# Performance work log

Measured on AMD Instinct MI355X. Metric: run time of the kernel, lower is better.

The kernel has to match this reference:

```python
import jax, jax.numpy as jnp
import numpy as np

NH, NKV, HD = 16, 4, 128
ROPE_THETA = 10000.0


def setup_inputs() -> dict:
    key = jax.random.key(0)
    ks = jax.random.split(key, 5)
    std = jnp.float32(0.02)
    return {
        "hidden_states": jax.random.normal(ks[0], (1, 2048, 2048), jnp.float32),
        "wq": jax.random.normal(ks[1], (2048, NH * HD), jnp.float32) * std,
        "wk": jax.random.normal(ks[2], (2048, NKV * HD), jnp.float32) * std,
        "wv": jax.random.normal(ks[3], (2048, NKV * HD), jnp.float32) * std,
        "wo": jax.random.normal(ks[4], (NH * HD, 2048), jnp.float32) * std,
    }


def _rope(x, cos, sin):
    # x: [B,S,n,hd]; pairs (even,odd) treated as complex, multiplied by cis(angle)
    xr = x.reshape(*x.shape[:-1], HD // 2, 2)
    re, im = xr[..., 0], xr[..., 1]
    c = cos[None, :, None, :]  # [1,S,1,hd/2]
    s = sin[None, :, None, :]
    out = jnp.stack((re * c - im * s, re * s + im * c), axis=-1)
    return out.reshape(x.shape)


def reference(hidden_states, wq, wk, wv, wo):
    B, S, H = hidden_states.shape
    q = (hidden_states @ wq).reshape(B, S, NH, HD)
    k = (hidden_states @ wk).reshape(B, S, NKV, HD)
    v = (hidden_states @ wv).reshape(B, S, NKV, HD)

    # precompute_freqs_cis (full rotary dim, rot_dim=None)
    freqs = 1.0 / (ROPE_THETA ** (jnp.arange(0, HD, 2, dtype=jnp.float32) / HD))
    ang = jnp.outer(jnp.arange(S, dtype=jnp.float32), freqs)  # [S, hd/2]
    cos, sin = jnp.cos(ang), jnp.sin(ang)

    q = _rope(q.astype(jnp.float32), cos, sin)
    k = _rope(k.astype(jnp.float32), cos, sin)

    # GQA: repeat_kv == repeat_interleave over head axis
    n_rep = NH // NKV
    k = jnp.repeat(k, n_rep, axis=2)  # [B,S,NH,HD]
    v = jnp.repeat(v, n_rep, axis=2)

    scale = jnp.float32(1.0 / np.sqrt(HD))
    scores = jnp.einsum("bqhd,bkhd->bhqk", q, k) * scale
    causal = jnp.tril(jnp.ones((S, S), dtype=bool))
    scores = jnp.where(causal[None, None], scores, jnp.float32(-1e9))
    attn = jax.nn.softmax(scores, axis=-1)
    out = jnp.einsum("bhqk,bkhd->bqhd", attn, v).reshape(B, S, NH * HD)
    return out @ wo
```

## Files before the change

kernel.cpp:

```cpp
#include <hip/hip_runtime.h>
#include <cstdint>

typedef __attribute__((ext_vector_type(8))) short short8;
typedef __attribute__((ext_vector_type(4))) float f32x4;

static __device__ __forceinline__ unsigned short f2bf(float x) {
  union { float f; unsigned int u; } c; c.f = x;
  unsigned int u = c.u;
  unsigned int r = (u + 0x7fffu + ((u >> 16) & 1u)) >> 16;
  return (unsigned short)r;
}

static __device__ __forceinline__ void gl_lds16(const void* g, void* l) {
  __builtin_amdgcn_global_load_lds((const __attribute__((address_space(1))) void*)g,
                                   (__attribute__((address_space(3))) void*)l, 16, 0, 0);
}

__global__ __launch_bounds__(256) void k_f32_to_bf16(const float* __restrict__ src,
                                                     unsigned short* __restrict__ dst,
                                                     int n4) {
  int i = blockIdx.x * 256 + threadIdx.x;
  if (i >= n4) return;
  float4 v = reinterpret_cast<const float4*>(src)[i];
  ushort4 o;
  o.x = f2bf(v.x); o.y = f2bf(v.y); o.z = f2bf(v.z); o.w = f2bf(v.w);
  reinterpret_cast<ushort4*>(dst)[i] = o;
}

__global__ __launch_bounds__(256) void k_transpose_bf16(const float* __restrict__ src,
                                                        unsigned short* __restrict__ dst,
                                                        int K, int N, int sstride) {
  __shared__ float tile[32][33];
  int bn = blockIdx.x * 32, bk = blockIdx.y * 32;
  int tx = threadIdx.x & 31, ty = threadIdx.x >> 5;
#pragma unroll
  for (int i = 0; i < 32; i += 8)
    tile[ty + i][tx] = src[(size_t)(bk + ty + i) * sstride + bn + tx];
  __syncthreads();
#pragma unroll
  for (int i = 0; i < 32; i += 8)
    dst[(size_t)(bn + ty + i) * K + bk + tx] = f2bf(tile[tx][ty + i]);
}

__global__ __launch_bounds__(256) void k_transpose_all(const float* __restrict__ wq,
                                                       const float* __restrict__ wk,
                                                       const float* __restrict__ wv,
                                                       const float* __restrict__ wo,
                                                       unsigned short* __restrict__ wqt,
                                                       unsigned short* __restrict__ wkt,
                                                       unsigned short* __restrict__ wvt,
                                                       unsigned short* __restrict__ wot) {
  __shared__ float tile[32][33];
  int id = blockIdx.x;
  const float* src; unsigned short* dst; int N, t;
  if (id < 4096)       { src = wq; dst = wqt; N = 2048; t = id; }
  else if (id < 8192)  { src = wo; dst = wot; N = 2048; t = id - 4096; }
  else if (id < 9216)  { src = wk; dst = wkt; N = 512;  t = id - 8192; }
  else                 { src = wv; dst = wvt; N = 512;  t = id - 9216; }
  const int K = 2048;
  int ntx = N >> 5;
  int bn = (t % ntx) * 32, bk = (t / ntx) * 32;
  int tx = threadIdx.x & 31, ty = threadIdx.x >> 5;
#pragma unroll
  for (int i = 0; i < 32; i += 8)
    tile[ty + i][tx] = src[(size_t)(bk + ty + i) * N + bn + tx];
  __syncthreads();
#pragma unroll
  for (int i = 0; i < 32; i += 8)
    dst[(size_t)(bn + ty + i) * K + bk + tx] = f2bf(tile[tx][ty + i]);
}

__global__ __launch_bounds__(256) void k_rope_fused(const float* __restrict__ qkvf,
                                                    unsigned short* __restrict__ qd,
                                                    unsigned short* __restrict__ kd) {
  int idx = blockIdx.x * 256 + threadIdx.x;
  int i = idx & 63;
  int hh = (idx >> 6) % 20;
  int s = idx / (64 * 20);
  float freq = powf(10000.0f, -(float)i / 64.0f);
  float ang = (float)s * freq;
  float sn, cs;
  sincosf(ang, &sn, &cs);
  size_t sb; unsigned short* dp; float amp;
  if (hh < 16) {
    int col = hh * 128 + 2 * i;
    sb = (size_t)s * 3072 + col;
    dp = qd + (size_t)s * 2048 + col;
    amp = 0.12751742836257666f;
  } else {
    int col = (hh - 16) * 128 + 2 * i;
    sb = (size_t)s * 3072 + 2048 + col;
    dp = kd + (size_t)s * 512 + col;
    amp = 1.0f;
  }
  float re = qkvf[sb] * amp, im = qkvf[sb + 1] * amp;
  unsigned int lo = f2bf(re * cs - im * sn);
  unsigned int hi = f2bf(re * sn + im * cs);
  *(unsigned int*)dp = lo | (hi << 16);
}

__global__ __launch_bounds__(256) void k_gemm_bf16(const unsigned short* __restrict__ A,
                                                   const unsigned short* __restrict__ Bt,
                                                   float* __restrict__ C,
                                                   int M, int N, int K) {
  __shared__ short sA[2][128 * 64];
  __shared__ short sB[2][64 * 64];
  int tid = threadIdx.x;
  int lane = tid & 63, wid = tid >> 6;
  int wr = wid >> 1, wc = wid & 1;

  int gx = gridDim.x, nwg = gx * gridDim.y;
  int flat = blockIdx.y * gx + blockIdx.x;
  int l = (flat & 7) * (nwg >> 3) + (flat >> 3);
  int bx = l % gx, by = l / gx;
  int m0 = by * 128, n0 = bx * 64;

  f32x4 acc[4][2] = {};

  int srcCol = (((tid & 7) ^ ((tid >> 3) & 7)) << 3);
  int rA = tid >> 3;
  const unsigned short* Ag = A + (size_t)(m0 + rA) * K + srcCol;
  const unsigned short* Bg = Bt + (size_t)(n0 + rA) * K + srcCol;
  int wb = (tid & ~63) * 8;

  int g = lane >> 4, fr = lane & 15, sw = fr & 7;

#define STAGE_G(buf, kof) do { \
    gl_lds16(Ag + (kof),                    &sA[buf][wb]); \
    gl_lds16(Ag + 32 * (size_t)K + (kof),   &sA[buf][2048 + wb]); \
    gl_lds16(Ag + 64 * (size_t)K + (kof),   &sA[buf][4096 + wb]); \
    gl_lds16(Ag + 96 * (size_t)K + (kof),   &sA[buf][6144 + wb]); \
    gl_lds16(Bg + (kof),                    &sB[buf][wb]); \
    gl_lds16(Bg + 32 * (size_t)K + (kof),   &sB[buf][2048 + wb]); \
  } while (0)

  int nt = K >> 6;
  STAGE_G(0, 0);
  __syncthreads();

  int cur = 0;
  for (int t = 0; t < nt; t++) {
    if (t + 1 < nt) STAGE_G(cur ^ 1, (size_t)((t + 1) << 6));
    const short* sAc = sA[cur];
    const short* sBc = sB[cur];
#pragma unroll
    for (int kk = 0; kk < 2; kk++) {
      int so = ((((kk << 2) + g) ^ sw) << 3);
      short8 af[4], bf2[2];
#pragma unroll
      for (int x = 0; x < 4; x++)
        af[x] = *(const short8*)(sAc + (wr * 64 + x * 16 + fr) * 64 + so);
#pragma unroll
      for (int ni = 0; ni < 2; ni++)
        bf2[ni] = *(const short8*)(sBc + (wc * 32 + ni * 16 + fr) * 64 + so);
#pragma unroll
      for (int x = 0; x < 4; x++)
#pragma unroll
        for (int ni = 0; ni < 2; ni++)
          acc[x][ni] = __builtin_amdgcn_mfma_f32_16x16x32_bf16(af[x], bf2[ni], acc[x][ni], 0, 0, 0);
    }
    __syncthreads();
    cur ^= 1;
  }
#undef STAGE_G

  int col = n0 + wc * 32 + fr;
  int rb = m0 + wr * 64 + (g << 2);
#pragma unroll
  for (int x = 0; x < 4; x++)
#pragma unroll
    for (int ni = 0; ni < 2; ni++)
#pragma unroll
      for (int j = 0; j < 4; j++)
        C[(size_t)(rb + x * 16 + j) * N + col + ni * 16] = acc[x][ni][j];
}

#define KSTR 136
#define VSTR 72
#define PSTR 72
__global__ __launch_bounds__(256) void k_attn_mfma(const unsigned short* __restrict__ Qb,
                                                   const unsigned short* __restrict__ Kb,
                                                   const unsigned short* __restrict__ Vt,
                                                   unsigned short* __restrict__ O) {
  __shared__ short sK[2][64 * KSTR];
  __shared__ short sV[2][128 * VSTR];
  __shared__ short sP[4][16 * PSTR];
  int h = blockIdx.y;
  int x = blockIdx.x;
  int qb = (h < 8) ? x : (31 - x);
  int q0 = qb * 64;
  int kvh = h >> 2;
  int tid = threadIdx.x, lane = tid & 63, w = tid >> 6;
  int fr = lane & 15, g = lane >> 4, kq = g << 3;

  short8 qf[4];
  {
    const unsigned short* qrow = Qb + (size_t)(q0 + w * 16 + fr) * 2048 + h * 128 + kq;
#pragma unroll
    for (int ko = 0; ko < 4; ko++) qf[ko] = *(const short8*)(qrow + ko * 32);
  }

  f32x4 oacc[8];
#pragma unroll
  for (int nd = 0; nd < 8; nd++) oacc[nd] = (f32x4){0.f, 0.f, 0.f, 0.f};
  float m_i = -3e38f;
  float l_i = 0.f;

  int skr = tid >> 2, skc = (tid & 3) << 5;
  int svd = tid >> 1, svc = (tid & 1) << 5;
  const unsigned short* Kbase = Kb + (size_t)kvh * 128 + skc;
  const unsigned short* Vbase = Vt + (size_t)(kvh * 128 + svd) * 2048 + svc;
  short* pw = (short*)sP[w];
  int kdOff = skr * KSTR + skc;
  int vdOff = svd * VSTR + svc;

  short8 kreg[4], vreg[4];
  {
    const short8* ks = (const short8*)(Kbase + (size_t)skr * 512);
    const short8* vs = (const short8*)(Vbase);
#pragma unroll
    for (int j = 0; j < 4; j++) { kreg[j] = ks[j]; vreg[j] = vs[j]; }
  }
  {
    short* kd = sK[0] + kdOff; short* vd = sV[0] + vdOff;
#pragma unroll
    for (int j = 0; j < 4; j++) { *(short8*)(kd + j * 8) = kreg[j]; *(short8*)(vd + j * 8) = vreg[j]; }
  }
  if (qb >= 1) {
    const short8* ks = (const short8*)(Kbase + (size_t)(64 + skr) * 512);
    const short8* vs = (const short8*)(Vbase + 64);
#pragma unroll
    for (int j = 0; j < 4; j++) { kreg[j] = ks[j]; vreg[j] = vs[j]; }
  }
  __syncthreads();

  int qrowS = q0 + w * 16 + fr;

  for (int kt = 0; kt <= qb; kt++) {
    int c = kt & 1;
    const short* sKc = sK[c];
    const short* sVc = sV[c];

    f32x4 sacc[4];
#pragma unroll
    for (int ni = 0; ni < 4; ni++) sacc[ni] = (f32x4){0.f, 0.f, 0.f, 0.f};
    __builtin_amdgcn_s_setprio(1);
#pragma unroll
    for (int ko = 0; ko < 4; ko++)
#pragma unroll
      for (int ni = 0; ni < 4; ni++) {
        short8 kf = *(const short8*)(sKc + (ni * 16 + fr) * KSTR + kq + ko * 32);
        sacc[ni] = __builtin_amdgcn_mfma_f32_16x16x32_bf16(kf, qf[ko], sacc[ni], 0, 0, 0);
      }
    __builtin_amdgcn_s_setprio(0);

    if (kt == qb) {
      int k0 = kt * 64;
#pragma unroll
      for (int ni = 0; ni < 4; ni++) {
        int kc = k0 + ni * 16 + (g << 2);
#pragma unroll
        for (int j = 0; j < 4; j++)
          if (kc + j > qrowS) sacc[ni][j] = -3e38f;
      }
    }

    float tm = sacc[0][0];
#pragma unroll
    for (int ni = 0; ni < 4; ni++)
#pragma unroll
      for (int j = 0; j < 4; j++) tm = fmaxf(tm, sacc[ni][j]);
    tm = fmaxf(tm, __shfl_xor(tm, 16));
    tm = fmaxf(tm, __shfl_xor(tm, 32));

    if (!__all(tm <= m_i + 8.0f)) {
      float mn = fmaxf(m_i, tm);
      float sc = exp2f(m_i - mn);
      m_i = mn;
      float scj[4];
#pragma unroll
      for (int j = 0; j < 4; j++) scj[j] = __shfl(sc, (g << 2) + j);
#pragma unroll
      for (int nd = 0; nd < 8; nd++)
#pragma unroll
        for (int j = 0; j < 4; j++) oacc[nd][j] *= scj[j];
      l_i *= sc;
    }

    float ps = 0.f;
#pragma unroll
    for (int ni = 0; ni < 4; ni++) {
      float p0 = exp2f(sacc[ni][0] - m_i);
      float p1 = exp2f(sacc[ni][1] - m_i);
      float p2 = exp2f(sacc[ni][2] - m_i);
      float p3 = exp2f(sacc[ni][3] - m_i);
      ps += (p0 + p1) + (p2 + p3);
      ushort4 pk;
      pk.x = f2bf(p0); pk.y = f2bf(p1); pk.z = f2bf(p2); pk.w = f2bf(p3);
      *(ushort4*)(pw + fr * PSTR + ni * 16 + (g << 2)) = pk;
    }
    ps += __shfl_xor(ps, 16);
    ps += __shfl_xor(ps, 32);
    l_i += ps;

    __builtin_amdgcn_s_setprio(1);
#pragma unroll
    for (int ks = 0; ks < 2; ks++) {
      short8 pa = *(const short8*)(pw + fr * PSTR + kq + ks * 32);
#pragma unroll
      for (int nd = 0; nd < 8; nd++) {
        short8 vb = *(const short8*)(sVc + (nd * 16 + fr) * VSTR + kq + ks * 32);
        oacc[nd] = __builtin_amdgcn_mfma_f32_16x16x32_bf16(pa, vb, oacc[nd], 0, 0, 0);
      }
    }
    __builtin_amdgcn_s_setprio(0);

    if (kt < qb) {
      short* kd = sK[c ^ 1] + kdOff; short* vd = sV[c ^ 1] + vdOff;
#pragma unroll
      for (int j = 0; j < 4; j++) { *(short8*)(kd + j * 8) = kreg[j]; *(short8*)(vd + j * 8) = vreg[j]; }
      if (kt + 1 < qb) {
        int k2 = (kt + 2) * 64;
        const short8* ks = (const short8*)(Kbase + (size_t)(k2 + skr) * 512);
        const short8* vs = (const short8*)(Vbase + k2);
#pragma unroll
        for (int j = 0; j < 4; j++) { kreg[j] = ks[j]; vreg[j] = vs[j]; }
      }
      __syncthreads();
    }
  }

  int orow = q0 + w * 16 + (g << 2);
#pragma unroll
  for (int j = 0; j < 4; j++) {
    float lj = __shfl(l_i, (g << 2) + j);
    float inv = 1.0f / lj;
#pragma unroll
    for (int nd = 0; nd < 8; nd++)
      O[(size_t)(orow + j) * 2048 + h * 128 + nd * 16 + fr] = f2bf(oacc[nd][j] * inv);
  }
}

extern "C" void kernel_launch(void* const* d_in, const int* in_sizes, int n_in,
                              void* d_out, int out_size, void* d_ws, size_t ws_size,
                              hipStream_t stream) {
  const float* hs = (const float*)d_in[0];
  const float* wq = (const float*)d_in[1];
  const float* wk = (const float*)d_in[2];
  const float* wv = (const float*)d_in[3];
  const float* wo = (const float*)d_in[4];
  char* ws = (char*)d_ws;

  unsigned short* hb   = (unsigned short*)(ws);
  unsigned short* wqt  = (unsigned short*)(ws + 8388608);
  unsigned short* wkt  = (unsigned short*)(ws + 16777216);
  unsigned short* wvt  = (unsigned short*)(ws + 18874368);
  unsigned short* wot  = (unsigned short*)(ws + 20971520);
  float* qkvf          = (float*)(ws + 29360128);
  unsigned short* q_bf = wqt;
  unsigned short* k_bf = wkt;
  unsigned short* vt_bf = wvt;
  unsigned short* ao   = hb;
  float* out = (float*)d_out;

  k_f32_to_bf16<<<4096, 256, 0, stream>>>(hs, hb, 2048 * 2048 / 4);
  k_transpose_all<<<10240, 256, 0, stream>>>(wq, wk, wv, wo, wqt, wkt, wvt, wot);

  k_gemm_bf16<<<dim3(48, 16), 256, 0, stream>>>(hb, wqt, qkvf, 2048, 3072, 2048);

  k_rope_fused<<<10240, 256, 0, stream>>>(qkvf, q_bf, k_bf);
  k_transpose_bf16<<<dim3(16, 64), 256, 0, stream>>>(qkvf + 2560, vt_bf, 2048, 512, 3072);

  k_attn_mfma<<<dim3(32, 16), 256, 0, stream>>>(q_bf, k_bf, vt_bf, ao);

  k_gemm_bf16<<<dim3(32, 16), 256, 0, stream>>>(ao, wot, out, 2048, 2048, 2048);
}
```

Before: 155.7 us.

## Enlarge GEMM tile, prefetch two stages ahead, fuse V transpose into QKV epilogue

The GEMM tile grows from 128x64 to 128x128, so each wave computes a 4x4 grid of MFMA fragments. The k-loop now issues global-to-LDS loads two tiles ahead, using explicit vmcnt waits and raw s_barriers in place of __syncthreads. The QKV GEMM epilogue writes the V columns directly as transposed bf16 into the V^T buffer, which removes the separate transpose kernel and its fp32 round trip. In exchange the block count halves, which can lower occupancy and wave balance on the output projection, and the hand-tuned waitcnt logic is fragile.

Result: slower. 161.7 us (+3.9%).

```diff
diff --git a/kernel.cpp b/kernel.cpp
--- a/kernel.cpp
+++ b/kernel.cpp
@@ -25,21 +25,6 @@
   ushort4 o;
   o.x = f2bf(v.x); o.y = f2bf(v.y); o.z = f2bf(v.z); o.w = f2bf(v.w);
   reinterpret_cast<ushort4*>(dst)[i] = o;
-}
-
-__global__ __launch_bounds__(256) void k_transpose_bf16(const float* __restrict__ src,
-                                                        unsigned short* __restrict__ dst,
-                                                        int K, int N, int sstride) {
-  __shared__ float tile[32][33];
-  int bn = blockIdx.x * 32, bk = blockIdx.y * 32;
-  int tx = threadIdx.x & 31, ty = threadIdx.x >> 5;
-#pragma unroll
-  for (int i = 0; i < 32; i += 8)
-    tile[ty + i][tx] = src[(size_t)(bk + ty + i) * sstride + bn + tx];
-  __syncthreads();
-#pragma unroll
-  for (int i = 0; i < 32; i += 8)
-    dst[(size_t)(bn + ty + i) * K + bk + tx] = f2bf(tile[tx][ty + i]);
 }
 
 __global__ __launch_bounds__(256) void k_transpose_all(const float* __restrict__ wq,
@@ -102,9 +87,10 @@
 __global__ __launch_bounds__(256) void k_gemm_bf16(const unsigned short* __restrict__ A,
                                                    const unsigned short* __restrict__ Bt,
                                                    float* __restrict__ C,
-                                                   int M, int N, int K) {
+                                                   unsigned short* __restrict__ VT,
+                                                   int M, int N, int K, int vcol0) {
   __shared__ short sA[2][128 * 64];
-  __shared__ short sB[2][64 * 64];
+  __shared__ short sB[2][128 * 64];
   int tid = threadIdx.x;
   int lane = tid & 63, wid = tid >> 6;
   int wr = wid >> 1, wc = wid & 1;
@@ -113,9 +99,9 @@
   int flat = blockIdx.y * gx + blockIdx.x;
   int l = (flat & 7) * (nwg >> 3) + (flat >> 3);
   int bx = l % gx, by = l / gx;
-  int m0 = by * 128, n0 = bx * 64;
-
-  f32x4 acc[4][2] = {};
+  int m0 = by * 128, n0 = bx * 128;
+
+  f32x4 acc[4][4] = {};
 
   int srcCol = (((tid & 7) ^ ((tid >> 3) & 7)) << 3);
   int rA = tid >> 3;
@@ -132,47 +118,67 @@
     gl_lds16(Ag + 96 * (size_t)K + (kof),   &sA[buf][6144 + wb]); \
     gl_lds16(Bg + (kof),                    &sB[buf][wb]); \
     gl_lds16(Bg + 32 * (size_t)K + (kof),   &sB[buf][2048 + wb]); \
+    gl_lds16(Bg + 64 * (size_t)K + (kof),   &sB[buf][4096 + wb]); \
+    gl_lds16(Bg + 96 * (size_t)K + (kof),   &sB[buf][6144 + wb]); \
   } while (0)
 
   int nt = K >> 6;
   STAGE_G(0, 0);
-  __syncthreads();
-
-  int cur = 0;
+  STAGE_G(1, 64);
+
   for (int t = 0; t < nt; t++) {
-    if (t + 1 < nt) STAGE_G(cur ^ 1, (size_t)((t + 1) << 6));
-    const short* sAc = sA[cur];
-    const short* sBc = sB[cur];
+    if (t < nt - 1) {
+      asm volatile("s_waitcnt vmcnt(8)" ::: "memory");
+    } else {
+      asm volatile("s_waitcnt vmcnt(0)" ::: "memory");
+    }
+    __builtin_amdgcn_sched_barrier(0);
+    __builtin_amdgcn_s_barrier();
+
+    const short* sAc = sA[t & 1];
+    const short* sBc = sB[t & 1];
 #pragma unroll
     for (int kk = 0; kk < 2; kk++) {
       int so = ((((kk << 2) + g) ^ sw) << 3);
-      short8 af[4], bf2[2];
+      short8 af[4], bf4[4];
 #pragma unroll
       for (int x = 0; x < 4; x++)
         af[x] = *(const short8*)(sAc + (wr * 64 + x * 16 + fr) * 64 + so);
 #pragma unroll
-      for (int ni = 0; ni < 2; ni++)
-        bf2[ni] = *(const short8*)(sBc + (wc * 32 + ni * 16 + fr) * 64 + so);
+      for (int ni = 0; ni < 4; ni++)
+        bf4[ni] = *(const short8*)(sBc + (wc * 64 + ni * 16 + fr) * 64 + so);
 #pragma unroll
       for (int x = 0; x < 4; x++)
 #pragma unroll
-        for (int ni = 0; ni < 2; ni++)
-          acc[x][ni] = __builtin_amdgcn_mfma_f32_16x16x32_bf16(af[x], bf2[ni], acc[x][ni], 0, 0, 0);
-    }
-    __syncthreads();
-    cur ^= 1;
+        for (int ni = 0; ni < 4; ni++)
+          acc[x][ni] = __builtin_amdgcn_mfma_f32_16x16x32_bf16(af[x], bf4[ni], acc[x][ni], 0, 0, 0);
+    }
+
+    __builtin_amdgcn_s_barrier();
+    if (t + 2 < nt) STAGE_G(t & 1, (size_t)((t + 2) << 6));
   }
 #undef STAGE_G
 
-  int col = n0 + wc * 32 + fr;
   int rb = m0 + wr * 64 + (g << 2);
 #pragma unroll
-  for (int x = 0; x < 4; x++)
-#pragma unroll
-    for (int ni = 0; ni < 2; ni++)
-#pragma unroll
-      for (int j = 0; j < 4; j++)
-        C[(size_t)(rb + x * 16 + j) * N + col + ni * 16] = acc[x][ni][j];
+  for (int ni = 0; ni < 4; ni++) {
+    int col = n0 + wc * 64 + ni * 16 + fr;
+    if (col >= vcol0) {
+#pragma unroll
+      for (int x = 0; x < 4; x++) {
+        ushort4 pk;
+        pk.x = f2bf(acc[x][ni][0]); pk.y = f2bf(acc[x][ni][1]);
+        pk.z = f2bf(acc[x][ni][2]); pk.w = f2bf(acc[x][ni][3]);
+        *(ushort4*)(VT + (size_t)(col - vcol0) * 2048 + rb + x * 16) = pk;
+      }
+    } else {
+#pragma unroll
+      for (int x = 0; x < 4; x++)
+#pragma unroll
+        for (int j = 0; j < 4; j++)
+          C[(size_t)(rb + x * 16 + j) * N + col] = acc[x][ni][j];
+    }
+  }
 }
 
 #define KSTR 136
@@ -366,12 +372,12 @@
   k_f32_to_bf16<<<4096, 256, 0, stream>>>(hs, hb, 2048 * 2048 / 4);
   k_transpose_all<<<10240, 256, 0, stream>>>(wq, wk, wv, wo, wqt, wkt, wvt, wot);
 
-  k_gemm_bf16<<<dim3(48, 16), 256, 0, stream>>>(hb, wqt, qkvf, 2048, 3072, 2048);
+  k_gemm_bf16<<<dim3(24, 16), 256, 0, stream>>>(hb, wqt, qkvf, vt_bf, 2048, 3072, 2048, 2560);
 
   k_rope_fused<<<10240, 256, 0, stream>>>(qkvf, q_bf, k_bf);
-  k_transpose_bf16<<<dim3(16, 64), 256, 0, stream>>>(qkvf + 2560, vt_bf, 2048, 512, 3072);
 
   k_attn_mfma<<<dim3(32, 16), 256, 0, stream>>>(q_bf, k_bf, vt_bf, ao);
 
-  k_gemm_bf16<<<dim3(32, 16), 256, 0, stream>>>(ao, wot, out, 2048, 2048, 2048);
-}
+  k_gemm_bf16<<<dim3(16, 16), 256, 0, stream>>>(ao, wot, out, (unsigned short*)nullptr,
+                                                2048, 2048, 2048, 1 << 30);
+}
```

## Fuse RoPE and V transpose into QKV GEMM epilogue with sincos table

Applied to the files above, without the earlier changes.

The QKV GEMM epilogue now writes bf16 Q and K with RoPE applied, pairing even and odd columns through lane shuffles, and writes V directly in transposed bf16 layout. This removes the fp32 qkv intermediate buffer and two separate kernels (rope and transpose), along with their memory round trips. A small precompute kernel builds a cos/sin table instead of evaluating sincos per element. In exchange the epilogue does scattered 2-byte stores and table loads, which may be poorly coalesced.

New measurement: 147.0 us. 1.06x faster.

```diff
diff --git a/kernel.cpp b/kernel.cpp
--- a/kernel.cpp
+++ b/kernel.cpp
@@ -14,6 +14,15 @@
 static __device__ __forceinline__ void gl_lds16(const void* g, void* l) {
   __builtin_amdgcn_global_load_lds((const __attribute__((address_space(1))) void*)g,
                                    (__attribute__((address_space(3))) void*)l, 16, 0, 0);
+}
+
+__global__ __launch_bounds__(256) void k_sincos(float2* __restrict__ ctab) {
+  int idx = blockIdx.x * 256 + threadIdx.x;
+  int s = idx >> 6, i = idx & 63;
+  float freq = powf(10000.0f, -(float)i / 64.0f);
+  float sn, cs;
+  sincosf((float)s * freq, &sn, &cs);
+  ctab[idx] = make_float2(cs, sn);
 }
 
 __global__ __launch_bounds__(256) void k_f32_to_bf16(const float* __restrict__ src,
@@ -25,21 +34,6 @@
   ushort4 o;
   o.x = f2bf(v.x); o.y = f2bf(v.y); o.z = f2bf(v.z); o.w = f2bf(v.w);
   reinterpret_cast<ushort4*>(dst)[i] = o;
-}
-
-__global__ __launch_bounds__(256) void k_transpose_bf16(const float* __restrict__ src,
-                                                        unsigned short* __restrict__ dst,
-                                                        int K, int N, int sstride) {
-  __shared__ float tile[32][33];
-  int bn = blockIdx.x * 32, bk = blockIdx.y * 32;
-  int tx = threadIdx.x & 31, ty = threadIdx.x >> 5;
-#pragma unroll
-  for (int i = 0; i < 32; i += 8)
-    tile[ty + i][tx] = src[(size_t)(bk + ty + i) * sstride + bn + tx];
-  __syncthreads();
-#pragma unroll
-  for (int i = 0; i < 32; i += 8)
-    dst[(size_t)(bn + ty + i) * K + bk + tx] = f2bf(tile[tx][ty + i]);
 }
 
 __global__ __launch_bounds__(256) void k_transpose_all(const float* __restrict__ wq,
@@ -70,39 +64,14 @@
     dst[(size_t)(bn + ty + i) * K + bk + tx] = f2bf(tile[tx][ty + i]);
 }
 
-__global__ __launch_bounds__(256) void k_rope_fused(const float* __restrict__ qkvf,
-                                                    unsigned short* __restrict__ qd,
-                                                    unsigned short* __restrict__ kd) {
-  int idx = blockIdx.x * 256 + threadIdx.x;
-  int i = idx & 63;
-  int hh = (idx >> 6) % 20;
-  int s = idx / (64 * 20);
-  float freq = powf(10000.0f, -(float)i / 64.0f);
-  float ang = (float)s * freq;
-  float sn, cs;
-  sincosf(ang, &sn, &cs);
-  size_t sb; unsigned short* dp; float amp;
-  if (hh < 16) {
-    int col = hh * 128 + 2 * i;
-    sb = (size_t)s * 3072 + col;
-    dp = qd + (size_t)s * 2048 + col;
-    amp = 0.12751742836257666f;
-  } else {
-    int col = (hh - 16) * 128 + 2 * i;
-    sb = (size_t)s * 3072 + 2048 + col;
-    dp = kd + (size_t)s * 512 + col;
-    amp = 1.0f;
-  }
-  float re = qkvf[sb] * amp, im = qkvf[sb + 1] * amp;
-  unsigned int lo = f2bf(re * cs - im * sn);
-  unsigned int hi = f2bf(re * sn + im * cs);
-  *(unsigned int*)dp = lo | (hi << 16);
-}
-
 __global__ __launch_bounds__(256) void k_gemm_bf16(const unsigned short* __restrict__ A,
                                                    const unsigned short* __restrict__ Bt,
                                                    float* __restrict__ C,
-                                                   int M, int N, int K) {
+                                                   unsigned short* __restrict__ Qd,
+                                                   unsigned short* __restrict__ Kd,
+                                                   unsigned short* __restrict__ VT,
+                                                   const float2* __restrict__ ctab,
+                                                   int M, int N, int K, int fuse) {
   __shared__ short sA[2][128 * 64];
   __shared__ short sB[2][64 * 64];
   int tid = threadIdx.x;
@@ -164,15 +133,57 @@
   }
 #undef STAGE_G
 
-  int col = n0 + wc * 32 + fr;
   int rb = m0 + wr * 64 + (g << 2);
-#pragma unroll
-  for (int x = 0; x < 4; x++)
-#pragma unroll
-    for (int ni = 0; ni < 2; ni++)
-#pragma unroll
-      for (int j = 0; j < 4; j++)
-        C[(size_t)(rb + x * 16 + j) * N + col + ni * 16] = acc[x][ni][j];
+  if (!fuse) {
+#pragma unroll
+    for (int ni = 0; ni < 2; ni++) {
+      int col = n0 + wc * 32 + ni * 16 + fr;
+#pragma unroll
+      for (int x = 0; x < 4; x++)
+#pragma unroll
+        for (int j = 0; j < 4; j++)
+          C[(size_t)(rb + x * 16 + j) * N + col] = acc[x][ni][j];
+    }
+    return;
+  }
+
+  const float QAMP = 0.12751742836257666f;
+#pragma unroll
+  for (int ni = 0; ni < 2; ni++) {
+    int col = n0 + wc * 32 + ni * 16 + fr;
+    if (col >= 2560) {
+#pragma unroll
+      for (int x = 0; x < 4; x++) {
+        ushort4 pk;
+        pk.x = f2bf(acc[x][ni][0]); pk.y = f2bf(acc[x][ni][1]);
+        pk.z = f2bf(acc[x][ni][2]); pk.w = f2bf(acc[x][ni][3]);
+        *(ushort4*)(VT + (size_t)(col - 2560) * 2048 + rb + x * 16) = pk;
+      }
+    } else {
+      int ipair = (col & 127) >> 1;
+      bool even = (col & 1) == 0;
+      bool isQ = col < 2048;
+      unsigned short* dst = isQ ? Qd : Kd;
+      int stride = isQ ? 2048 : 512;
+      int dcol = isQ ? col : (col - 2048);
+      float amp = isQ ? QAMP : 1.0f;
+#pragma unroll
+      for (int x = 0; x < 4; x++) {
+        f32x4 a = acc[x][ni];
+        float p0 = __shfl_xor(a[0], 1), p1 = __shfl_xor(a[1], 1);
+        float p2 = __shfl_xor(a[2], 1), p3 = __shfl_xor(a[3], 1);
+        float pv[4] = {p0, p1, p2, p3};
+#pragma unroll
+        for (int j = 0; j < 4; j++) {
+          int r = rb + x * 16 + j;
+          float2 cs = ctab[r * 64 + ipair];
+          float o = even ? (a[j] * cs.x - pv[j] * cs.y)
+                         : (pv[j] * cs.y + a[j] * cs.x);
+          dst[(size_t)r * stride + dcol] = f2bf(o * amp);
+        }
+      }
+    }
+  }
 }
 
 #define KSTR 136
@@ -356,22 +367,27 @@
   unsigned short* wkt  = (unsigned short*)(ws + 16777216);
   unsigned short* wvt  = (unsigned short*)(ws + 18874368);
   unsigned short* wot  = (unsigned short*)(ws + 20971520);
-  float* qkvf          = (float*)(ws + 29360128);
-  unsigned short* q_bf = wqt;
-  unsigned short* k_bf = wkt;
-  unsigned short* vt_bf = wvt;
+  unsigned short* q_bf = (unsigned short*)(ws + 29360128);
+  unsigned short* k_bf = (unsigned short*)(ws + 37748736);
+  unsigned short* vt_bf= (unsigned short*)(ws + 39845888);
+  float2* ctab         = (float2*)(ws + 41943040);
   unsigned short* ao   = hb;
   float* out = (float*)d_out;
 
+  k_sincos<<<512, 256, 0, stream>>>(ctab);
   k_f32_to_bf16<<<4096, 256, 0, stream>>>(hs, hb, 2048 * 2048 / 4);
   k_transpose_all<<<10240, 256, 0, stream>>>(wq, wk, wv, wo, wqt, wkt, wvt, wot);
 
-  k_gemm_bf16<<<dim3(48, 16), 256, 0, stream>>>(hb, wqt, qkvf, 2048, 3072, 2048);
-
-  k_rope_fused<<<10240, 256, 0, stream>>>(qkvf, q_bf, k_bf);
-  k_transpose_bf16<<<dim3(16, 64), 256, 0, stream>>>(qkvf + 2560, vt_bf, 2048, 512, 3072);
+  k_gemm_bf16<<<dim3(48, 16), 256, 0, stream>>>(hb, wqt, (float*)nullptr,
+                                                q_bf, k_bf, vt_bf, ctab,
+                                                2048, 3072, 2048, 1);
 
   k_attn_mfma<<<dim3(32, 16), 256, 0, stream>>>(q_bf, k_bf, vt_bf, ao);
 
-  k_gemm_bf16<<<dim3(32, 16), 256, 0, stream>>>(ao, wot, out, 2048, 2048, 2048);
-}
+  k_gemm_bf16<<<dim3(32, 16), 256, 0, stream>>>(ao, wot, out,
+                                                (unsigned short*)nullptr,
+                                                (unsigned short*)nullptr,
+                                                (unsigned short*)nullptr,
+                                                (const float2*)nullptr,
+                                                2048, 2048, 2048, 0);
+}
```
